# Kernel tuning notes

Hardware: AMD Instinct MI355X
Metric: run time of the kernel (lower is better)

## Reference

```python
import jax, jax.numpy as jnp
import numpy as np

N_NODES = 50000
N_EDGES = 800000
IN_DIM = 256
OUT_DIM = 256


def setup_inputs() -> dict:
    key = jax.random.key(0)
    k1, k2, k3, k4, k5, k6 = jax.random.split(key, 6)
    x = jax.random.normal(k1, (N_NODES, IN_DIM), dtype=jnp.float32)
    adj_rows = jax.random.randint(k2, (N_EDGES,), 0, N_NODES)
    adj_cols = jax.random.randint(k3, (N_EDGES,), 0, N_NODES)
    adj_vals = jax.random.uniform(k4, (N_EDGES,), dtype=jnp.float32)
    stdv = 1.0 / np.sqrt(OUT_DIM)
    W = jax.random.uniform(k5, (IN_DIM, OUT_DIM), minval=-stdv, maxval=stdv, dtype=jnp.float32)
    b = jax.random.uniform(k6, (OUT_DIM,), minval=-stdv, maxval=stdv, dtype=jnp.float32)
    return {"x": x, "adj_rows": adj_rows, "adj_cols": adj_cols, "adj_vals": adj_vals, "W": W, "b": b}


def reference(x, adj_rows, adj_cols, adj_vals, W, b):
    # hidden = x @ W  (first sparse.mm; x treated dense, identical math)
    hidden = jnp.matmul(x, W)  # [N, out_dim]
    # output = adj @ hidden via COO SpMM: gather source rows, scale, scatter-add to dest rows
    msgs = adj_vals[:, None] * hidden[adj_cols]  # [E, out_dim]
    output = jax.ops.segment_sum(msgs, adj_rows, num_segments=N_NODES)  # [N, out_dim]
    return output + b
```

## Files before the change

kernel.cpp:

```cpp
#include <hip/hip_runtime.h>

#define N_NODES 50000
#define N_EDGES 800000
#define DIM     256
#define STRIPS32 1563
#define NBLK_NODES 196
#define GEMM_BLOCKS 196

typedef __attribute__((ext_vector_type(8))) short bf16x8;
typedef __attribute__((ext_vector_type(4))) float f32x4;

__device__ __forceinline__ unsigned short f2bf(float f) {
    unsigned u = __float_as_uint(f);
    unsigned r = (u + 0x7fffu + ((u >> 16) & 1u)) >> 16;
    return (unsigned short)r;
}
__device__ __forceinline__ float bf2f(unsigned short h) {
    return __uint_as_float((unsigned)h << 16);
}

__device__ __forceinline__ int block_excl_scan_256(int v, int* wsum, int* total) {
    const int lane = threadIdx.x & 63;
    const int wave = threadIdx.x >> 6;
    int x = v;
#pragma unroll
    for (int off = 1; off < 64; off <<= 1) {
        const int y = __shfl_up(x, off, 64);
        if (lane >= off) x += y;
    }
    if (lane == 63) wsum[wave] = x;
    __syncthreads();
    if (threadIdx.x == 0) {
        int s = 0;
#pragma unroll
        for (int w = 0; w < 4; ++w) { const int t = wsum[w]; wsum[w] = s; s += t; }
        *total = s;
    }
    __syncthreads();
    return wsum[wave] + x - v;
}

__global__ __launch_bounds__(256)
void prep(const float* __restrict__ W, unsigned short* __restrict__ Wt,
          int* __restrict__ cnt) {
    const int i = blockIdx.x * 256 + threadIdx.x;
    if (i < N_NODES) cnt[i] = 0;
    const int n = blockIdx.x, k = threadIdx.x;
    Wt[n * DIM + k] = f2bf(W[(size_t)k * DIM + n]);
}

__global__ __launch_bounds__(512, 2)
void gemm_mfma(const float* __restrict__ X, const unsigned short* __restrict__ Wt,
               unsigned short* __restrict__ Hb) {
    __shared__ unsigned short wl[DIM * DIM];
    const int tid = threadIdx.x;
    {
        const uint4* src = (const uint4*)Wt;
#pragma unroll
        for (int i = 0; i < 16; ++i) {
            const int c   = i * 512 + tid;
            const int row = c >> 5;
            const int kb  = (c & 31) * 16;
            const int dst = row * 512 + (kb ^ ((row & 7) << 4));
            *(uint4*)((char*)wl + dst) = src[c];
        }
    }
    __syncthreads();

    const int wid   = tid >> 6;
    const int lane  = tid & 63;
    const int strip = blockIdx.x * 8 + wid;
    if (strip >= STRIPS32) return;

    const int r0   = strip * 32;
    const int arow = lane & 15;
    const int kgrp = lane >> 4;
    const int ra = r0 + arow;
    const int rb = r0 + 16 + arow;
    const float* xa = X + (size_t)(ra < N_NODES ? ra : N_NODES - 1) * DIM + kgrp * 8;
    const float* xb = X + (size_t)(rb < N_NODES ? rb : N_NODES - 1) * DIM + kgrp * 8;

    f32x4 acc[2][16];
#pragma unroll
    for (int h = 0; h < 2; ++h)
#pragma unroll
        for (int nt = 0; nt < 16; ++nt) acc[h][nt] = f32x4{0.f, 0.f, 0.f, 0.f};

    const int swz = (arow & 7) << 4;

    float4 pa0 = *(const float4*)(xa);
    float4 pa1 = *(const float4*)(xa + 4);
    float4 pb0 = *(const float4*)(xb);
    float4 pb1 = *(const float4*)(xb + 4);

#pragma unroll
    for (int ks = 0; ks < 8; ++ks) {
        bf16x8 a0, a1;
        a0[0] = (short)f2bf(pa0.x); a0[1] = (short)f2bf(pa0.y);
        a0[2] = (short)f2bf(pa0.z); a0[3] = (short)f2bf(pa0.w);
        a0[4] = (short)f2bf(pa1.x); a0[5] = (short)f2bf(pa1.y);
        a0[6] = (short)f2bf(pa1.z); a0[7] = (short)f2bf(pa1.w);
        a1[0] = (short)f2bf(pb0.x); a1[1] = (short)f2bf(pb0.y);
        a1[2] = (short)f2bf(pb0.z); a1[3] = (short)f2bf(pb0.w);
        a1[4] = (short)f2bf(pb1.x); a1[5] = (short)f2bf(pb1.y);
        a1[6] = (short)f2bf(pb1.z); a1[7] = (short)f2bf(pb1.w);
        if (ks < 7) {
            pa0 = *(const float4*)(xa + (ks + 1) * 32);
            pa1 = *(const float4*)(xa + (ks + 1) * 32 + 4);
            pb0 = *(const float4*)(xb + (ks + 1) * 32);
            pb1 = *(const float4*)(xb + (ks + 1) * 32 + 4);
        }
        const int kb = ((ks * 32 + kgrp * 8) * 2) ^ swz;
#pragma unroll
        for (int nt = 0; nt < 16; ++nt) {
            const int n = nt * 16 + arow;
            const bf16x8 b = *(const bf16x8*)((const char*)wl + n * 512 + kb);
            acc[0][nt] = __builtin_amdgcn_mfma_f32_16x16x32_bf16(a0, b, acc[0][nt], 0, 0, 0);
            acc[1][nt] = __builtin_amdgcn_mfma_f32_16x16x32_bf16(a1, b, acc[1][nt], 0, 0, 0);
        }
    }

#pragma unroll
    for (int h = 0; h < 2; ++h) {
        const int crow0 = r0 + h * 16 + kgrp * 4;
#pragma unroll
        for (int nt = 0; nt < 16; ++nt) {
#pragma unroll
            for (int q = 0; q < 4; ++q) {
                const int r = crow0 + q;
                if (r < N_NODES)
                    Hb[(size_t)r * DIM + nt * 16 + arow] = f2bf(acc[h][nt][q]);
            }
        }
    }
}

__global__ __launch_bounds__(256)
void count_rank(const int* __restrict__ rows, int* __restrict__ cnt,
                unsigned short* __restrict__ rank) {
    const int e0 = (blockIdx.x * 256 + threadIdx.x) * 4;
    if (e0 >= N_EDGES) return;
    const int4 r4 = *(const int4*)&rows[e0];
    ushort4 rk;
    rk.x = (unsigned short)atomicAdd(&cnt[r4.x], 1);
    rk.y = (unsigned short)atomicAdd(&cnt[r4.y], 1);
    rk.z = (unsigned short)atomicAdd(&cnt[r4.z], 1);
    rk.w = (unsigned short)atomicAdd(&cnt[r4.w], 1);
    *(ushort4*)&rank[e0] = rk;
}

__global__ __launch_bounds__(256)
void scan_blocks(const int* __restrict__ cnt, int* __restrict__ offs,
                 int* __restrict__ bsum) {
    __shared__ int wsum[4];
    __shared__ int total;
    const int i = blockIdx.x * 256 + threadIdx.x;
    const int v = (i < N_NODES) ? cnt[i] : 0;
    const int excl = block_excl_scan_256(v, wsum, &total);
    if (i < N_NODES) offs[i] = excl;
    if (threadIdx.x == 0) bsum[blockIdx.x] = total;
}

__global__ __launch_bounds__(256)
void fill_edges(const int* __restrict__ rows, const int* __restrict__ cols,
                const float* __restrict__ vals, const int* __restrict__ offs,
                const int* __restrict__ bsum, const unsigned short* __restrict__ rank,
                int2* __restrict__ pe) {
    __shared__ int wsum[4];
    __shared__ int total;
    __shared__ int P[256];
    {
        const int t = threadIdx.x;
        const int v = (t < NBLK_NODES) ? bsum[t] : 0;
        const int excl = block_excl_scan_256(v, wsum, &total);
        P[t] = excl;
    }
    __syncthreads();
    const int e = blockIdx.x * 256 + threadIdx.x;
    if (e >= N_EDGES) return;
    const int r = rows[e];
    pe[offs[r] + P[r >> 8] + rank[e]] = make_int2(cols[e], __float_as_int(vals[e]));
}

__global__ __launch_bounds__(256)
void spmm(const unsigned short* __restrict__ Hb, const int* __restrict__ offs,
          const int* __restrict__ bsum, const int2* __restrict__ pe,
          const float* __restrict__ bias, float* __restrict__ out) {
    __shared__ int wsum[4];
    __shared__ int total;
    __shared__ int P[256];
    {
        const int t = threadIdx.x;
        const int v = (t < NBLK_NODES) ? bsum[t] : 0;
        const int excl = block_excl_scan_256(v, wsum, &total);
        P[t] = excl;
    }
    __syncthreads();

    const int row  = blockIdx.x * 4 + (threadIdx.x >> 6);
    const int lane = threadIdx.x & 63;
    const int beg = offs[row] + P[row >> 8];
    const int end = (row + 1 == N_NODES) ? N_EDGES : (offs[row + 1] + P[(row + 1) >> 8]);
    const unsigned lb = (unsigned)lane * 4;
    float4 acc = make_float4(0.f, 0.f, 0.f, 0.f);
    int i = beg;
    for (; i + 8 <= end; i += 8) {
        int2 e[8];
#pragma unroll
        for (int j = 0; j < 8; ++j) e[j] = pe[i + j];
        ushort4 h[8];
#pragma unroll
        for (int j = 0; j < 8; ++j)
            h[j] = *(const ushort4*)&Hb[((unsigned)e[j].x << 8) + lb];
#pragma unroll
        for (int j = 0; j < 8; ++j) {
            const float v = __int_as_float(e[j].y);
            acc.x += v * bf2f(h[j].x);
            acc.y += v * bf2f(h[j].y);
            acc.z += v * bf2f(h[j].z);
            acc.w += v * bf2f(h[j].w);
        }
    }
    for (; i < end; ++i) {
        const int2 e0 = pe[i];
        const ushort4 h0 = *(const ushort4*)&Hb[((unsigned)e0.x << 8) + lb];
        const float v0 = __int_as_float(e0.y);
        acc.x += v0 * bf2f(h0.x);
        acc.y += v0 * bf2f(h0.y);
        acc.z += v0 * bf2f(h0.z);
        acc.w += v0 * bf2f(h0.w);
    }
    const float4 bb = *(const float4*)&bias[lane * 4];
    acc.x += bb.x; acc.y += bb.y; acc.z += bb.z; acc.w += bb.w;
    *(float4*)&out[(size_t)row * DIM + lane * 4] = acc;
}

extern "C" void kernel_launch(void* const* d_in, const int* in_sizes, int n_in,
                              void* d_out, int out_size, void* d_ws, size_t ws_size,
                              hipStream_t stream) {
    const float* x        = (const float*)d_in[0];
    const int*   adj_rows = (const int*)d_in[1];
    const int*   adj_cols = (const int*)d_in[2];
    const float* adj_vals = (const float*)d_in[3];
    const float* W        = (const float*)d_in[4];
    const float* b        = (const float*)d_in[5];
    float*       out      = (float*)d_out;

    char* ws = (char*)d_ws;
    size_t off = 0;
    auto alloc = [&](size_t bytes) {
        void* p = ws + off;
        off = (off + bytes + 255) & ~(size_t)255;
        return p;
    };
    unsigned short* hiddenb = (unsigned short*)alloc((size_t)N_NODES * DIM * sizeof(unsigned short));
    unsigned short* Wt      = (unsigned short*)alloc((size_t)DIM * DIM * sizeof(unsigned short));
    int*            offs    = (int*)alloc((size_t)N_NODES * sizeof(int));
    int*            cnt     = (int*)alloc((size_t)N_NODES * sizeof(int));
    int*            bsum    = (int*)alloc(256 * sizeof(int));
    unsigned short* rank    = (unsigned short*)alloc((size_t)N_EDGES * sizeof(unsigned short));
    int2*           pe      = (int2*)alloc((size_t)N_EDGES * sizeof(int2));

    prep<<<DIM, 256, 0, stream>>>(W, Wt, cnt);

    gemm_mfma<<<GEMM_BLOCKS, 512, 0, stream>>>(x, Wt, hiddenb);

    count_rank<<<(N_EDGES / 4 + 255) / 256, 256, 0, stream>>>(adj_rows, cnt, rank);

    scan_blocks<<<NBLK_NODES, 256, 0, stream>>>(cnt, offs, bsum);

    fill_edges<<<(N_EDGES + 255) / 256, 256, 0, stream>>>(
        adj_rows, adj_cols, adj_vals, offs, bsum, rank, pe);

    spmm<<<N_NODES / 4, 256, 0, stream>>>(hiddenb, offs, bsum, pe, b, out);
}
```

Before: 245.3 us.

## Fuse all stages into one persistent kernel with software grid barriers

```diff
diff --git a/kernel.cpp b/kernel.cpp
--- a/kernel.cpp
+++ b/kernel.cpp
@@ -3,9 +3,12 @@
 #define N_NODES 50000
 #define N_EDGES 800000
 #define DIM     256
-#define STRIPS32 1563
+#define NSTRIPS 1563
+#define GRID    256
+#define NT      512
+#define NWAVES  (GRID * 8)
+#define CNT_THREADS ((NWAVES - NSTRIPS) * 64)
 #define NBLK_NODES 196
-#define GEMM_BLOCKS 196
 
 typedef __attribute__((ext_vector_type(8))) short bf16x8;
 typedef __attribute__((ext_vector_type(4))) float f32x4;
@@ -19,7 +22,19 @@
     return __uint_as_float((unsigned)h << 16);
 }
 
-__device__ __forceinline__ int block_excl_scan_256(int v, int* wsum, int* total) {
+__device__ __forceinline__ void gridbar(unsigned* bar, unsigned target) {
+    __syncthreads();
+    if (threadIdx.x == 0) {
+        __threadfence();
+        atomicAdd(bar, 1u);
+        while (__hip_atomic_load(bar, __ATOMIC_RELAXED, __HIP_MEMORY_SCOPE_AGENT) < target)
+            __builtin_amdgcn_s_sleep(2);
+        __threadfence();
+    }
+    __syncthreads();
+}
+
+__device__ __forceinline__ int excl_scan_512(int v, int* wsum, int* totalp) {
     const int lane = threadIdx.x & 63;
     const int wave = threadIdx.x >> 6;
     int x = v;
@@ -33,206 +48,182 @@
     if (threadIdx.x == 0) {
         int s = 0;
 #pragma unroll
-        for (int w = 0; w < 4; ++w) { const int t = wsum[w]; wsum[w] = s; s += t; }
-        *total = s;
+        for (int w = 0; w < 8; ++w) { const int t = wsum[w]; wsum[w] = s; s += t; }
+        *totalp = s;
     }
     __syncthreads();
     return wsum[wave] + x - v;
 }
 
-__global__ __launch_bounds__(256)
-void prep(const float* __restrict__ W, unsigned short* __restrict__ Wt,
-          int* __restrict__ cnt) {
-    const int i = blockIdx.x * 256 + threadIdx.x;
-    if (i < N_NODES) cnt[i] = 0;
-    const int n = blockIdx.x, k = threadIdx.x;
-    Wt[n * DIM + k] = f2bf(W[(size_t)k * DIM + n]);
-}
-
-__global__ __launch_bounds__(512, 2)
-void gemm_mfma(const float* __restrict__ X, const unsigned short* __restrict__ Wt,
-               unsigned short* __restrict__ Hb) {
-    __shared__ unsigned short wl[DIM * DIM];
-    const int tid = threadIdx.x;
+__global__ __launch_bounds__(NT, 2)
+void fused(const float* __restrict__ X, const float* __restrict__ W,
+           const int* __restrict__ rows, const int* __restrict__ cols,
+           const float* __restrict__ vals, const float* __restrict__ bias,
+           unsigned short* __restrict__ Hb, int* __restrict__ offs,
+           int* __restrict__ cnt, unsigned* __restrict__ bar,
+           int* __restrict__ bsum, unsigned short* __restrict__ rank,
+           int2* __restrict__ pe, float* __restrict__ out) {
+    __shared__ union {
+        unsigned short wl[DIM * DIM];
+        int P[256];
+    } sh;
+    __shared__ int s_wsum[8];
+    __shared__ int s_total;
+
+    const int tid  = threadIdx.x;
+    const int bid  = blockIdx.x;
+    const int lane = tid & 63;
+    const int wid  = tid >> 6;
+    const int gw   = bid * 8 + wid;
+
+    if (bid < NBLK_NODES) {
+        const int n = tid >> 1;
+        const int khalf = tid & 1;
+#pragma unroll
+        for (int j8 = 0; j8 < 16; ++j8) {
+            const int k0 = khalf * 128 + j8 * 8;
+            bf16x8 v;
+#pragma unroll
+            for (int i = 0; i < 8; ++i)
+                v[i] = (short)f2bf(W[(size_t)(k0 + i) * DIM + n]);
+            const int byteoff = n * 512 + ((k0 * 2) ^ ((n & 7) << 4));
+            *(bf16x8*)((char*)sh.wl + byteoff) = v;
+        }
+        __syncthreads();
+    }
+
+    if (gw < NSTRIPS) {
+        const int r0   = gw * 32;
+        const int arow = lane & 15;
+        const int kgrp = lane >> 4;
+        const int ra = r0 + arow;
+        const int rb = r0 + 16 + arow;
+        const float* xa = X + (size_t)(ra < N_NODES ? ra : N_NODES - 1) * DIM + kgrp * 8;
+        const float* xb = X + (size_t)(rb < N_NODES ? rb : N_NODES - 1) * DIM + kgrp * 8;
+
+        f32x4 acc[2][16];
+#pragma unroll
+        for (int h = 0; h < 2; ++h)
+#pragma unroll
+            for (int nt = 0; nt < 16; ++nt) acc[h][nt] = f32x4{0.f, 0.f, 0.f, 0.f};
+
+        const int swz = (arow & 7) << 4;
+        float4 pa0 = *(const float4*)(xa);
+        float4 pa1 = *(const float4*)(xa + 4);
+        float4 pb0 = *(const float4*)(xb);
+        float4 pb1 = *(const float4*)(xb + 4);
+
+#pragma unroll
+        for (int ks = 0; ks < 8; ++ks) {
+            bf16x8 a0, a1;
+            a0[0] = (short)f2bf(pa0.x); a0[1] = (short)f2bf(pa0.y);
+            a0[2] = (short)f2bf(pa0.z); a0[3] = (short)f2bf(pa0.w);
+            a0[4] = (short)f2bf(pa1.x); a0[5] = (short)f2bf(pa1.y);
+            a0[6] = (short)f2bf(pa1.z); a0[7] = (short)f2bf(pa1.w);
+            a1[0] = (short)f2bf(pb0.x); a1[1] = (short)f2bf(pb0.y);
+            a1[2] = (short)f2bf(pb0.z); a1[3] = (short)f2bf(pb0.w);
+            a1[4] = (short)f2bf(pb1.x); a1[5] = (short)f2bf(pb1.y);
+            a1[6] = (short)f2bf(pb1.z); a1[7] = (short)f2bf(pb1.w);
+            if (ks < 7) {
+                pa0 = *(const float4*)(xa + (ks + 1) * 32);
+                pa1 = *(const float4*)(xa + (ks + 1) * 32 + 4);
+                pb0 = *(const float4*)(xb + (ks + 1) * 32);
+                pb1 = *(const float4*)(xb + (ks + 1) * 32 + 4);
+            }
+            const int kb = ((ks * 32 + kgrp * 8) * 2) ^ swz;
+#pragma unroll
+            for (int nt = 0; nt < 16; ++nt) {
+                const int n = nt * 16 + arow;
+                const bf16x8 b = *(const bf16x8*)((const char*)sh.wl + n * 512 + kb);
+                acc[0][nt] = __builtin_amdgcn_mfma_f32_16x16x32_bf16(a0, b, acc[0][nt], 0, 0, 0);
+                acc[1][nt] = __builtin_amdgcn_mfma_f32_16x16x32_bf16(a1, b, acc[1][nt], 0, 0, 0);
+            }
+        }
+#pragma unroll
+        for (int h = 0; h < 2; ++h) {
+            const int crow0 = r0 + h * 16 + kgrp * 4;
+#pragma unroll
+            for (int nt = 0; nt < 16; ++nt) {
+#pragma unroll
+                for (int q = 0; q < 4; ++q) {
+                    const int r = crow0 + q;
+                    if (r < N_NODES)
+                        Hb[(size_t)r * DIM + nt * 16 + arow] = f2bf(acc[h][nt][q]);
+                }
+            }
+        }
+    } else {
+        const int ct = (gw - NSTRIPS) * 64 + lane;
+        for (int e = ct; e < N_EDGES; e += CNT_THREADS) {
+            const int r = rows[e];
+            rank[e] = (unsigned short)atomicAdd(&cnt[r], 1);
+        }
+    }
+    gridbar(bar, GRID);
+
+    if (bid < NBLK_NODES) {
+        const int idx = bid * 256 + tid;
+        const int v = (tid < 256 && idx < N_NODES) ? cnt[idx] : 0;
+        const int excl = excl_scan_512(v, s_wsum, &s_total);
+        if (tid < 256 && idx < N_NODES) offs[idx] = excl;
+        if (tid == 0) bsum[bid] = s_total;
+    }
+    gridbar(bar, 2 * GRID);
+
     {
-        const uint4* src = (const uint4*)Wt;
-#pragma unroll
-        for (int i = 0; i < 16; ++i) {
-            const int c   = i * 512 + tid;
-            const int row = c >> 5;
-            const int kb  = (c & 31) * 16;
-            const int dst = row * 512 + (kb ^ ((row & 7) << 4));
-            *(uint4*)((char*)wl + dst) = src[c];
-        }
-    }
-    __syncthreads();
-
-    const int wid   = tid >> 6;
-    const int lane  = tid & 63;
-    const int strip = blockIdx.x * 8 + wid;
-    if (strip >= STRIPS32) return;
-
-    const int r0   = strip * 32;
-    const int arow = lane & 15;
-    const int kgrp = lane >> 4;
-    const int ra = r0 + arow;
-    const int rb = r0 + 16 + arow;
-    const float* xa = X + (size_t)(ra < N_NODES ? ra : N_NODES - 1) * DIM + kgrp * 8;
-    const float* xb = X + (size_t)(rb < N_NODES ? rb : N_NODES - 1) * DIM + kgrp * 8;
-
-    f32x4 acc[2][16];
-#pragma unroll
-    for (int h = 0; h < 2; ++h)
-#pragma unroll
-        for (int nt = 0; nt < 16; ++nt) acc[h][nt] = f32x4{0.f, 0.f, 0.f, 0.f};
-
-    const int swz = (arow & 7) << 4;
-
-    float4 pa0 = *(const float4*)(xa);
-    float4 pa1 = *(const float4*)(xa + 4);
-    float4 pb0 = *(const float4*)(xb);
-    float4 pb1 = *(const float4*)(xb + 4);
-
-#pragma unroll
-    for (int ks = 0; ks < 8; ++ks) {
-        bf16x8 a0, a1;
-        a0[0] = (short)f2bf(pa0.x); a0[1] = (short)f2bf(pa0.y);
-        a0[2] = (short)f2bf(pa0.z); a0[3] = (short)f2bf(pa0.w);
-        a0[4] = (short)f2bf(pa1.x); a0[5] = (short)f2bf(pa1.y);
-        a0[6] = (short)f2bf(pa1.z); a0[7] = (short)f2bf(pa1.w);
-        a1[0] = (short)f2bf(pb0.x); a1[1] = (short)f2bf(pb0.y);
-        a1[2] = (short)f2bf(pb0.z); a1[3] = (short)f2bf(pb0.w);
-        a1[4] = (short)f2bf(pb1.x); a1[5] = (short)f2bf(pb1.y);
-        a1[6] = (short)f2bf(pb1.z); a1[7] = (short)f2bf(pb1.w);
-        if (ks < 7) {
-            pa0 = *(const float4*)(xa + (ks + 1) * 32);
-            pa1 = *(const float4*)(xa + (ks + 1) * 32 + 4);
-            pb0 = *(const float4*)(xb + (ks + 1) * 32);
-            pb1 = *(const float4*)(xb + (ks + 1) * 32 + 4);
-        }
-        const int kb = ((ks * 32 + kgrp * 8) * 2) ^ swz;
-#pragma unroll
-        for (int nt = 0; nt < 16; ++nt) {
-            const int n = nt * 16 + arow;
-            const bf16x8 b = *(const bf16x8*)((const char*)wl + n * 512 + kb);
-            acc[0][nt] = __builtin_amdgcn_mfma_f32_16x16x32_bf16(a0, b, acc[0][nt], 0, 0, 0);
-            acc[1][nt] = __builtin_amdgcn_mfma_f32_16x16x32_bf16(a1, b, acc[1][nt], 0, 0, 0);
-        }
-    }
-
-#pragma unroll
-    for (int h = 0; h < 2; ++h) {
-        const int crow0 = r0 + h * 16 + kgrp * 4;
-#pragma unroll
-        for (int nt = 0; nt < 16; ++nt) {
-#pragma unroll
-            for (int q = 0; q < 4; ++q) {
-                const int r = crow0 + q;
-                if (r < N_NODES)
-                    Hb[(size_t)r * DIM + nt * 16 + arow] = f2bf(acc[h][nt][q]);
-            }
-        }
-    }
-}
-
-__global__ __launch_bounds__(256)
-void count_rank(const int* __restrict__ rows, int* __restrict__ cnt,
-                unsigned short* __restrict__ rank) {
-    const int e0 = (blockIdx.x * 256 + threadIdx.x) * 4;
-    if (e0 >= N_EDGES) return;
-    const int4 r4 = *(const int4*)&rows[e0];
-    ushort4 rk;
-    rk.x = (unsigned short)atomicAdd(&cnt[r4.x], 1);
-    rk.y = (unsigned short)atomicAdd(&cnt[r4.y], 1);
-    rk.z = (unsigned short)atomicAdd(&cnt[r4.z], 1);
-    rk.w = (unsigned short)atomicAdd(&cnt[r4.w], 1);
-    *(ushort4*)&rank[e0] = rk;
-}
-
-__global__ __launch_bounds__(256)
-void scan_blocks(const int* __restrict__ cnt, int* __restrict__ offs,
-                 int* __restrict__ bsum) {
-    __shared__ int wsum[4];
-    __shared__ int total;
-    const int i = blockIdx.x * 256 + threadIdx.x;
-    const int v = (i < N_NODES) ? cnt[i] : 0;
-    const int excl = block_excl_scan_256(v, wsum, &total);
-    if (i < N_NODES) offs[i] = excl;
-    if (threadIdx.x == 0) bsum[blockIdx.x] = total;
-}
-
-__global__ __launch_bounds__(256)
-void fill_edges(const int* __restrict__ rows, const int* __restrict__ cols,
-                const float* __restrict__ vals, const int* __restrict__ offs,
-                const int* __restrict__ bsum, const unsigned short* __restrict__ rank,
-                int2* __restrict__ pe) {
-    __shared__ int wsum[4];
-    __shared__ int total;
-    __shared__ int P[256];
+        const int v = (tid < NBLK_NODES) ? bsum[tid] : 0;
+        const int excl = excl_scan_512(v, s_wsum, &s_total);
+        if (tid < 256) sh.P[tid] = excl;
+    }
+    __syncthreads();
+    for (int e = bid * NT + tid; e < N_EDGES; e += GRID * NT) {
+        const int r = rows[e];
+        pe[offs[r] + sh.P[r >> 8] + (int)rank[e]] =
+            make_int2(cols[e], __float_as_int(vals[e]));
+    }
+    gridbar(bar, 3 * GRID);
+
     {
-        const int t = threadIdx.x;
-        const int v = (t < NBLK_NODES) ? bsum[t] : 0;
-        const int excl = block_excl_scan_256(v, wsum, &total);
-        P[t] = excl;
-    }
-    __syncthreads();
-    const int e = blockIdx.x * 256 + threadIdx.x;
-    if (e >= N_EDGES) return;
-    const int r = rows[e];
-    pe[offs[r] + P[r >> 8] + rank[e]] = make_int2(cols[e], __float_as_int(vals[e]));
-}
-
-__global__ __launch_bounds__(256)
-void spmm(const unsigned short* __restrict__ Hb, const int* __restrict__ offs,
-          const int* __restrict__ bsum, const int2* __restrict__ pe,
-          const float* __restrict__ bias, float* __restrict__ out) {
-    __shared__ int wsum[4];
-    __shared__ int total;
-    __shared__ int P[256];
-    {
-        const int t = threadIdx.x;
-        const int v = (t < NBLK_NODES) ? bsum[t] : 0;
-        const int excl = block_excl_scan_256(v, wsum, &total);
-        P[t] = excl;
-    }
-    __syncthreads();
-
-    const int row  = blockIdx.x * 4 + (threadIdx.x >> 6);
-    const int lane = threadIdx.x & 63;
-    const int beg = offs[row] + P[row >> 8];
-    const int end = (row + 1 == N_NODES) ? N_EDGES : (offs[row + 1] + P[(row + 1) >> 8]);
-    const unsigned lb = (unsigned)lane * 4;
-    float4 acc = make_float4(0.f, 0.f, 0.f, 0.f);
-    int i = beg;
-    for (; i + 8 <= end; i += 8) {
-        int2 e[8];
-#pragma unroll
-        for (int j = 0; j < 8; ++j) e[j] = pe[i + j];
-        ushort4 h[8];
-#pragma unroll
-        for (int j = 0; j < 8; ++j)
-            h[j] = *(const ushort4*)&Hb[((unsigned)e[j].x << 8) + lb];
-#pragma unroll
-        for (int j = 0; j < 8; ++j) {
-            const float v = __int_as_float(e[j].y);
-            acc.x += v * bf2f(h[j].x);
-            acc.y += v * bf2f(h[j].y);
-            acc.z += v * bf2f(h[j].z);
-            acc.w += v * bf2f(h[j].w);
-        }
-    }
-    for (; i < end; ++i) {
-        const int2 e0 = pe[i];
-        const ushort4 h0 = *(const ushort4*)&Hb[((unsigned)e0.x << 8) + lb];
-        const float v0 = __int_as_float(e0.y);
-        acc.x += v0 * bf2f(h0.x);
-        acc.y += v0 * bf2f(h0.y);
-        acc.z += v0 * bf2f(h0.z);
-        acc.w += v0 * bf2f(h0.w);
-    }
-    const float4 bb = *(const float4*)&bias[lane * 4];
-    acc.x += bb.x; acc.y += bb.y; acc.z += bb.z; acc.w += bb.w;
-    *(float4*)&out[(size_t)row * DIM + lane * 4] = acc;
+        const unsigned lb = (unsigned)lane * 4;
+        const float4 bb = *(const float4*)&bias[lane * 4];
+        for (int r = gw; r < N_NODES; r += NWAVES) {
+            const int beg = offs[r] + sh.P[r >> 8];
+            const int end = (r + 1 == N_NODES) ? N_EDGES
+                                               : (offs[r + 1] + sh.P[(r + 1) >> 8]);
+            float4 acc = make_float4(0.f, 0.f, 0.f, 0.f);
+            int i = beg;
+            for (; i + 8 <= end; i += 8) {
+                int2 e[8];
+#pragma unroll
+                for (int j = 0; j < 8; ++j) e[j] = pe[i + j];
+                ushort4 h[8];
+#pragma unroll
+                for (int j = 0; j < 8; ++j)
+                    h[j] = *(const ushort4*)&Hb[((unsigned)e[j].x << 8) + lb];
+#pragma unroll
+                for (int j = 0; j < 8; ++j) {
+                    const float v = __int_as_float(e[j].y);
+                    acc.x += v * bf2f(h[j].x);
+                    acc.y += v * bf2f(h[j].y);
+                    acc.z += v * bf2f(h[j].z);
+                    acc.w += v * bf2f(h[j].w);
+                }
+            }
+            for (; i < end; ++i) {
+                const int2 e0 = pe[i];
+                const ushort4 h0 = *(const ushort4*)&Hb[((unsigned)e0.x << 8) + lb];
+                const float v0 = __int_as_float(e0.y);
+                acc.x += v0 * bf2f(h0.x);
+                acc.y += v0 * bf2f(h0.y);
+                acc.z += v0 * bf2f(h0.z);
+                acc.w += v0 * bf2f(h0.w);
+            }
+            float4 o;
+            o.x = acc.x + bb.x; o.y = acc.y + bb.y;
+            o.z = acc.z + bb.z; o.w = acc.w + bb.w;
+            *(float4*)&out[(size_t)r * DIM + lane * 4] = o;
+        }
+    }
 }
 
 extern "C" void kernel_launch(void* const* d_in, const int* in_sizes, int n_in,
@@ -253,24 +244,17 @@
         off = (off + bytes + 255) & ~(size_t)255;
         return p;
     };
-    unsigned short* hiddenb = (unsigned short*)alloc((size_t)N_NODES * DIM * sizeof(unsigned short));
-    unsigned short* Wt      = (unsigned short*)alloc((size_t)DIM * DIM * sizeof(unsigned short));
+    unsigned short* hiddenb = (unsigned short*)alloc((size_t)N_NODES * DIM * 2);
     int*            offs    = (int*)alloc((size_t)N_NODES * sizeof(int));
-    int*            cnt     = (int*)alloc((size_t)N_NODES * sizeof(int));
+    int*            cntbar  = (int*)alloc((size_t)N_NODES * sizeof(int) + 64);
     int*            bsum    = (int*)alloc(256 * sizeof(int));
-    unsigned short* rank    = (unsigned short*)alloc((size_t)N_EDGES * sizeof(unsigned short));
+    unsigned short* rank    = (unsigned short*)alloc((size_t)N_EDGES * 2);
     int2*           pe      = (int2*)alloc((size_t)N_EDGES * sizeof(int2));
-
-    prep<<<DIM, 256, 0, stream>>>(W, Wt, cnt);
-
-    gemm_mfma<<<GEMM_BLOCKS, 512, 0, stream>>>(x, Wt, hiddenb);
-
-    count_rank<<<(N_EDGES / 4 + 255) / 256, 256, 0, stream>>>(adj_rows, cnt, rank);
-
-    scan_blocks<<<NBLK_NODES, 256, 0, stream>>>(cnt, offs, bsum);
-
-    fill_edges<<<(N_EDGES + 255) / 256, 256, 0, stream>>>(
-        adj_rows, adj_cols, adj_vals, offs, bsum, rank, pe);
-
-    spmm<<<N_NODES / 4, 256, 0, stream>>>(hiddenb, offs, bsum, pe, b, out);
-}
+    int*      cnt = cntbar;
+    unsigned* bar = (unsigned*)(cntbar + N_NODES);
+
+    hipMemsetAsync(cntbar, 0, (size_t)N_NODES * sizeof(int) + 64, stream);
+
+    fused<<<GRID, NT, 0, stream>>>(x, W, adj_rows, adj_cols, adj_vals, b,
+                                   hiddenb, offs, cnt, bar, bsum, rank, pe, out);
+}
```

New measurement: 343.4 us. 1.4x slower.

## Fuse W transpose with edge counting, precompute absolute offsets, split SpMM launch

Applied to the files above, without the earlier changes.

```diff
diff --git a/kernel.cpp b/kernel.cpp
--- a/kernel.cpp
+++ b/kernel.cpp
@@ -3,9 +3,12 @@
 #define N_NODES 50000
 #define N_EDGES 800000
 #define DIM     256
-#define STRIPS32 1563
+#define NSTRIPS 1563
 #define NBLK_NODES 196
 #define GEMM_BLOCKS 196
+#define PREP_BLOCKS 256
+#define CNT_BLOCKS 3125
+#define HALF_ROWS 25000
 
 typedef __attribute__((ext_vector_type(8))) short bf16x8;
 typedef __attribute__((ext_vector_type(4))) float f32x4;
@@ -41,12 +44,18 @@
 }
 
 __global__ __launch_bounds__(256)
-void prep(const float* __restrict__ W, unsigned short* __restrict__ Wt,
-          int* __restrict__ cnt) {
-    const int i = blockIdx.x * 256 + threadIdx.x;
-    if (i < N_NODES) cnt[i] = 0;
-    const int n = blockIdx.x, k = threadIdx.x;
-    Wt[n * DIM + k] = f2bf(W[(size_t)k * DIM + n]);
+void prep_count(const float* __restrict__ W, unsigned short* __restrict__ Wt,
+                const int* __restrict__ rows, int* __restrict__ cnt,
+                unsigned short* __restrict__ rank) {
+    const int bid = blockIdx.x;
+    if (bid < PREP_BLOCKS) {
+        const int n = bid, k = threadIdx.x;
+        Wt[n * DIM + k] = f2bf(W[(size_t)k * DIM + n]);
+        return;
+    }
+    const int e = (bid - PREP_BLOCKS) * 256 + threadIdx.x;
+    if (e < N_EDGES)
+        rank[e] = (unsigned short)atomicAdd(&cnt[rows[e]], 1);
 }
 
 __global__ __launch_bounds__(512, 2)
@@ -70,7 +79,7 @@
     const int wid   = tid >> 6;
     const int lane  = tid & 63;
     const int strip = blockIdx.x * 8 + wid;
-    if (strip >= STRIPS32) return;
+    if (strip >= NSTRIPS) return;
 
     const int r0   = strip * 32;
     const int arow = lane & 15;
@@ -87,7 +96,6 @@
         for (int nt = 0; nt < 16; ++nt) acc[h][nt] = f32x4{0.f, 0.f, 0.f, 0.f};
 
     const int swz = (arow & 7) << 4;
-
     float4 pa0 = *(const float4*)(xa);
     float4 pa1 = *(const float4*)(xa + 4);
     float4 pb0 = *(const float4*)(xb);
@@ -119,7 +127,6 @@
             acc[1][nt] = __builtin_amdgcn_mfma_f32_16x16x32_bf16(a1, b, acc[1][nt], 0, 0, 0);
         }
     }
-
 #pragma unroll
     for (int h = 0; h < 2; ++h) {
         const int crow0 = r0 + h * 16 + kgrp * 4;
@@ -133,20 +140,6 @@
             }
         }
     }
-}
-
-__global__ __launch_bounds__(256)
-void count_rank(const int* __restrict__ rows, int* __restrict__ cnt,
-                unsigned short* __restrict__ rank) {
-    const int e0 = (blockIdx.x * 256 + threadIdx.x) * 4;
-    if (e0 >= N_EDGES) return;
-    const int4 r4 = *(const int4*)&rows[e0];
-    ushort4 rk;
-    rk.x = (unsigned short)atomicAdd(&cnt[r4.x], 1);
-    rk.y = (unsigned short)atomicAdd(&cnt[r4.y], 1);
-    rk.z = (unsigned short)atomicAdd(&cnt[r4.z], 1);
-    rk.w = (unsigned short)atomicAdd(&cnt[r4.w], 1);
-    *(ushort4*)&rank[e0] = rk;
 }
 
 __global__ __launch_bounds__(256)
@@ -165,7 +158,7 @@
 void fill_edges(const int* __restrict__ rows, const int* __restrict__ cols,
                 const float* __restrict__ vals, const int* __restrict__ offs,
                 const int* __restrict__ bsum, const unsigned short* __restrict__ rank,
-                int2* __restrict__ pe) {
+                int2* __restrict__ pe, int* __restrict__ offs_abs) {
     __shared__ int wsum[4];
     __shared__ int total;
     __shared__ int P[256];
@@ -176,31 +169,26 @@
         P[t] = excl;
     }
     __syncthreads();
-    const int e = blockIdx.x * 256 + threadIdx.x;
+    const int bid = blockIdx.x;
+    if (bid < NBLK_NODES) {
+        const int i = bid * 256 + threadIdx.x;
+        if (i < N_NODES) offs_abs[i] = offs[i] + P[bid];
+        if (bid == 0 && threadIdx.x == 0) offs_abs[N_NODES] = N_EDGES;
+    }
+    const int e = bid * 256 + threadIdx.x;
     if (e >= N_EDGES) return;
     const int r = rows[e];
-    pe[offs[r] + P[r >> 8] + rank[e]] = make_int2(cols[e], __float_as_int(vals[e]));
-}
-
-__global__ __launch_bounds__(256)
-void spmm(const unsigned short* __restrict__ Hb, const int* __restrict__ offs,
-          const int* __restrict__ bsum, const int2* __restrict__ pe,
-          const float* __restrict__ bias, float* __restrict__ out) {
-    __shared__ int wsum[4];
-    __shared__ int total;
-    __shared__ int P[256];
-    {
-        const int t = threadIdx.x;
-        const int v = (t < NBLK_NODES) ? bsum[t] : 0;
-        const int excl = block_excl_scan_256(v, wsum, &total);
-        P[t] = excl;
-    }
-    __syncthreads();
-
-    const int row  = blockIdx.x * 4 + (threadIdx.x >> 6);
+    pe[offs[r] + P[r >> 8] + (int)rank[e]] = make_int2(cols[e], __float_as_int(vals[e]));
+}
+
+__global__ __launch_bounds__(256)
+void spmm(const unsigned short* __restrict__ Hb, const int* __restrict__ offs_abs,
+          const int2* __restrict__ pe, const float* __restrict__ bias,
+          float* __restrict__ out, int row_base) {
+    const int row  = row_base + blockIdx.x * 4 + (threadIdx.x >> 6);
     const int lane = threadIdx.x & 63;
-    const int beg = offs[row] + P[row >> 8];
-    const int end = (row + 1 == N_NODES) ? N_EDGES : (offs[row + 1] + P[(row + 1) >> 8]);
+    const int beg = offs_abs[row];
+    const int end = offs_abs[row + 1];
     const unsigned lb = (unsigned)lane * 4;
     float4 acc = make_float4(0.f, 0.f, 0.f, 0.f);
     int i = beg;
@@ -253,24 +241,26 @@
         off = (off + bytes + 255) & ~(size_t)255;
         return p;
     };
-    unsigned short* hiddenb = (unsigned short*)alloc((size_t)N_NODES * DIM * sizeof(unsigned short));
-    unsigned short* Wt      = (unsigned short*)alloc((size_t)DIM * DIM * sizeof(unsigned short));
-    int*            offs    = (int*)alloc((size_t)N_NODES * sizeof(int));
-    int*            cnt     = (int*)alloc((size_t)N_NODES * sizeof(int));
-    int*            bsum    = (int*)alloc(256 * sizeof(int));
-    unsigned short* rank    = (unsigned short*)alloc((size_t)N_EDGES * sizeof(unsigned short));
-    int2*           pe      = (int2*)alloc((size_t)N_EDGES * sizeof(int2));
-
-    prep<<<DIM, 256, 0, stream>>>(W, Wt, cnt);
+    unsigned short* hiddenb  = (unsigned short*)alloc((size_t)N_NODES * DIM * 2);
+    unsigned short* Wt       = (unsigned short*)alloc((size_t)DIM * DIM * 2);
+    int*            offs     = (int*)alloc((size_t)N_NODES * sizeof(int));
+    int*            offs_abs = (int*)alloc((size_t)(N_NODES + 1) * sizeof(int));
+    int*            cnt      = (int*)alloc((size_t)N_NODES * sizeof(int));
+    int*            bsum     = (int*)alloc(256 * sizeof(int));
+    unsigned short* rank     = (unsigned short*)alloc((size_t)N_EDGES * 2);
+    int2*           pe       = (int2*)alloc((size_t)N_EDGES * sizeof(int2));
+
+    hipMemsetAsync(cnt, 0, (size_t)N_NODES * sizeof(int), stream);
+
+    prep_count<<<PREP_BLOCKS + CNT_BLOCKS, 256, 0, stream>>>(W, Wt, adj_rows, cnt, rank);
 
     gemm_mfma<<<GEMM_BLOCKS, 512, 0, stream>>>(x, Wt, hiddenb);
 
-    count_rank<<<(N_EDGES / 4 + 255) / 256, 256, 0, stream>>>(adj_rows, cnt, rank);
-
     scan_blocks<<<NBLK_NODES, 256, 0, stream>>>(cnt, offs, bsum);
 
-    fill_edges<<<(N_EDGES + 255) / 256, 256, 0, stream>>>(
-        adj_rows, adj_cols, adj_vals, offs, bsum, rank, pe);
-
-    spmm<<<N_NODES / 4, 256, 0, stream>>>(hiddenb, offs, bsum, pe, b, out);
-}
+    fill_edges<<<CNT_BLOCKS, 256, 0, stream>>>(
+        adj_rows, adj_cols, adj_vals, offs, bsum, rank, pe, offs_abs);
+
+    spmm<<<HALF_ROWS / 4, 256, 0, stream>>>(hiddenb, offs_abs, pe, b, out, 0);
+    spmm<<<HALF_ROWS / 4, 256, 0, stream>>>(hiddenb, offs_abs, pe, b, out, HALF_ROWS);
+}
```

Measured after the change: 246.7 us. Within noise of the previous version (+0.6%).
